# Performance work log

Measured on AMD Instinct MI355X. Metric: run time of the kernel, lower is better.

## Reference

```python
import jax, jax.numpy as jnp
import numpy as np
import math

INV = 1.0 / (2.0 * math.pi) ** 2  # 1/(2*pi)^2 normalization used throughout
EPS = 1e-8


def setup_inputs() -> dict:
    key = jax.random.key(0)
    ks = jax.random.split(key, 5)
    N, K, J = 512, 8, 6
    return {
        "x_hat": jax.random.normal(ks[0], (N, N, 2), jnp.float32),
        "phi_hat_real": jax.random.normal(ks[1], (N, N), jnp.float32),
        "phi_hat_imag": jax.random.normal(ks[2], (N, N), jnp.float32),
        "psi_hat_real": jax.random.normal(ks[3], (K, J, N, N), jnp.float32),
        "psi_hat_imag": jax.random.normal(ks[4], (K, J, N, N), jnp.float32),
    }


def reference(x_hat, phi_hat_real, phi_hat_imag, psi_hat_real, psi_hat_imag):
    K, J, N, _ = psi_hat_real.shape
    NN = N * N
    phi2 = phi_hat_real ** 2 + phi_hat_imag ** 2  # [N,N]

    # zeroth-order coefficient: full spatial mean of |x_hat|^2 * |phi_hat|^2
    s0 = INV * jnp.mean((x_hat[:, :, 0] ** 2 + x_hat[:, :, 1] ** 2) * phi2)

    # first layer: complex multiply in Fourier domain, ifft2, modulus, fft2
    xc = jax.lax.complex(x_hat[:, :, 0], x_hat[:, :, 1])          # [N,N] complex
    psic = jax.lax.complex(psi_hat_real, psi_hat_imag)            # [K,J,N,N] complex
    temp = jnp.fft.ifft2(xc[None, None] * psic, axes=(-2, -1))    # [K,J,N,N] complex
    mod = jnp.sqrt(temp.real ** 2 + temp.imag ** 2 + EPS)         # modulus nonlinearity
    t2 = jnp.fft.fft2(mod, axes=(-2, -1))                         # rfft onesided=False == full fft of real
    power = (t2.real ** 2 + t2.imag ** 2).reshape(K, J, NN)       # |U1_hat|^2

    # first-order coefficients a[k,i] = INV * mean(power * phi2)
    a = INV * (power @ phi2.reshape(NN)) / NN                     # [K,J]

    # second-order coefficients via GEMM over spatial dim:
    # B[k,i,m,j] = INV * mean_xy(power[k,i] * |psi[m,j]|^2)
    psi2 = (psi_hat_real ** 2 + psi_hat_imag ** 2).reshape(K, J, NN)
    B = INV * jnp.einsum('kin,mjn->kimj', power, psi2) / NN       # [K,J,K,J]

    # assemble output in the same concatenation order as the torch loop:
    # [s0, a_0, b_0(flattened over k,m,j'), a_1, b_1, ..., a_{J-1}]
    pieces = [s0[None]]
    for i in range(J):
        pieces.append(a[:, i])
        if i < J - 1:
            pieces.append(B[:, i, :, i + 1:J].reshape(-1))
    return jnp.concatenate(pieces, axis=0)
```

## Files before the change

kernel.cpp:

```cpp
#include <hip/hip_runtime.h>
#include <hip/hip_fp16.h>

#define Nn 512
#define NNe 262144
#define CST 546

__device__ __forceinline__ float2 f2(float x, float y){ return make_float2(x, y); }
__device__ __forceinline__ float2 cadd(float2 a, float2 b){ return f2(a.x+b.x, a.y+b.y); }
__device__ __forceinline__ float2 csub(float2 a, float2 b){ return f2(a.x-b.x, a.y-b.y); }
__device__ __forceinline__ float2 cmul(float2 a, float2 b){
    return f2(a.x*b.x - a.y*b.y, a.x*b.y + a.y*b.x);
}
__device__ __forceinline__ int pidx(int p){ return p + (p>>4) + (p>>7); }
#define WFENCE() __builtin_amdgcn_wave_barrier()

template<int SGN>
__device__ __forceinline__ void fft8(float2 a[8]){
    const float r = 0.7071067811865476f;
    const float S = (float)SGN;
    float2 u0 = cadd(a[0], a[4]), u1 = cadd(a[1], a[5]);
    float2 u2 = cadd(a[2], a[6]), u3 = cadd(a[3], a[7]);
    float2 v0 = csub(a[0], a[4]), v1 = csub(a[1], a[5]);
    float2 v2 = csub(a[2], a[6]), v3 = csub(a[3], a[7]);
    v1 = cmul(v1, f2(r, S*r));
    v2 = cmul(v2, f2(0.f, S));
    v3 = cmul(v3, f2(-r, S*r));
    float2 p0 = cadd(u0, u2), p1 = cadd(u1, u3);
    float2 q0 = csub(u0, u2), q1 = cmul(csub(u1, u3), f2(0.f, S));
    a[0] = cadd(p0, p1); a[4] = csub(p0, p1);
    a[2] = cadd(q0, q1); a[6] = csub(q0, q1);
    p0 = cadd(v0, v2); p1 = cadd(v1, v3);
    q0 = csub(v0, v2); q1 = cmul(csub(v1, v3), f2(0.f, S));
    a[1] = cadd(p0, p1); a[5] = csub(p0, p1);
    a[3] = cadd(q0, q1); a[7] = csub(q0, q1);
}

template<int SGN>
__device__ __forceinline__ float2 twd(int idx, float inv){
    float ang = ((float)SGN) * 6.283185307179586f * (inv * (float)idx);
    float s, c;
    __sincosf(ang, &s, &c);
    return f2(c, s);
}

template<int SGN>
__device__ void fft512_dif(float2 v[8], float2* buf, int lane){
    fft8<SGN>(v);
    {
        float2 w1 = twd<SGN>(lane, 1.f/512.f);
        float2 w  = f2(1.f, 0.f);
        #pragma unroll
        for (int r = 0; r < 8; ++r){
            buf[pidx(r*64 + lane)] = cmul(v[r], w);
            w = cmul(w, w1);
        }
    }
    WFENCE();
    int rb = (lane >> 3) * 64, t2 = lane & 7;
    float2 y[8];
    #pragma unroll
    for (int q = 0; q < 8; ++q) y[q] = buf[pidx(rb + t2 + 8*q)];
    fft8<SGN>(y);
    WFENCE();
    {
        float2 w2 = twd<SGN>(t2, 1.f/64.f);
        float2 w  = f2(1.f, 0.f);
        #pragma unroll
        for (int r = 0; r < 8; ++r){
            buf[pidx(rb + r*8 + t2)] = cmul(y[r], w);
            w = cmul(w, w2);
        }
    }
    WFENCE();
    int base = rb + t2*8;
    #pragma unroll
    for (int q = 0; q < 8; ++q) v[q] = buf[pidx(base + q)];
    fft8<SGN>(v);
}

template<int SGN>
__device__ void fft512_dit(float2 v[8], float2* buf, int lane){
    int rb = (lane >> 3) * 64, t2 = lane & 7;
    fft8<SGN>(v);
    int base = rb + t2*8;
    #pragma unroll
    for (int q = 0; q < 8; ++q) buf[pidx(base + q)] = v[q];
    WFENCE();
    float2 y[8];
    #pragma unroll
    for (int r = 0; r < 8; ++r) y[r] = buf[pidx(rb + r*8 + t2)];
    {
        float2 w2 = twd<SGN>(t2, 1.f/64.f);
        float2 w  = f2(1.f, 0.f);
        #pragma unroll
        for (int r = 0; r < 8; ++r){
            y[r] = cmul(y[r], w);
            w = cmul(w, w2);
        }
    }
    fft8<SGN>(y);
    WFENCE();
    #pragma unroll
    for (int q = 0; q < 8; ++q) buf[pidx(rb + t2 + 8*q)] = y[q];
    WFENCE();
    #pragma unroll
    for (int r = 0; r < 8; ++r) v[r] = buf[pidx(r*64 + lane)];
    {
        float2 w1 = twd<SGN>(lane, 1.f/512.f);
        float2 w  = f2(1.f, 0.f);
        #pragma unroll
        for (int r = 0; r < 8; ++r){
            v[r] = cmul(v[r], w);
            w = cmul(w, w1);
        }
    }
    fft8<SGN>(v);
}

__global__ __launch_bounds__(256, 6)
void k_mulrow(const float2* __restrict__ xh, const float* __restrict__ pr,
              const float* __restrict__ pi, __half2* __restrict__ temp,
              __half* __restrict__ psi2h){
    __shared__ float2 lds[4][548];
    int wave = threadIdx.x >> 6, lane = threadIdx.x & 63;
    int img  = blockIdx.x >> 7;
    int row  = ((blockIdx.x & 127) << 2) | wave;
    size_t boff = (size_t)img * NNe + (size_t)row * Nn;
    const float2* xr = xh + (size_t)row * Nn;
    float2 v[8];
    #pragma unroll
    for (int q = 0; q < 8; ++q){
        int x = lane + 64*q;
        float2 xv = xr[x];
        float2 pv = f2(pr[boff + x], pi[boff + x]);
        psi2h[boff + x] = __float2half_rn(pv.x*pv.x + pv.y*pv.y);
        v[q] = cmul(xv, pv);
    }
    fft512_dif<1>(v, lds[wave], lane);
    __half2* outp = temp + boff;
    #pragma unroll
    for (int q = 0; q < 8; ++q) outp[64*q + lane] = __floats2half2_rn(v[q].x, v[q].y);
}

__global__ __launch_bounds__(512, 6)
void k_colfused(__half2* __restrict__ temp){
    __shared__ float2 tile[8 * CST];
    int img = blockIdx.x >> 6;
    int x0  = (blockIdx.x & 63) << 3;
    __half2* srcH = temp + (size_t)img * NNe + x0;
    for (int i = threadIdx.x; i < 1024; i += 512){
        int yy = i >> 1, c4 = (i & 1) << 2;
        uint4 u = *(const uint4*)&srcH[(size_t)yy * Nn + c4];
        tile[(c4+0)*CST + pidx(yy)] = __half22float2(*(__half2*)&u.x);
        tile[(c4+1)*CST + pidx(yy)] = __half22float2(*(__half2*)&u.y);
        tile[(c4+2)*CST + pidx(yy)] = __half22float2(*(__half2*)&u.z);
        tile[(c4+3)*CST + pidx(yy)] = __half22float2(*(__half2*)&u.w);
    }
    __syncthreads();
    int wave = threadIdx.x >> 6, lane = threadIdx.x & 63;
    const float sc = 3.814697265625e-06f;
    {
        float2* buf = &tile[wave * CST];
        float2 v[8];
        #pragma unroll
        for (int q = 0; q < 8; ++q) v[q] = buf[pidx(lane + 64*q)];
        fft512_dif<1>(v, buf, lane);
        #pragma unroll
        for (int q = 0; q < 8; ++q){
            float re = v[q].x * sc, im = v[q].y * sc;
            v[q] = f2(sqrtf(re*re + im*im + 1e-8f), 0.f);
        }
        WFENCE();
        fft512_dit<-1>(v, buf, lane);
        #pragma unroll
        for (int q = 0; q < 8; ++q) buf[pidx(lane + 64*q)] = v[q];
    }
    __syncthreads();
    for (int i = threadIdx.x; i < 1024; i += 512){
        int yy = i >> 1, c4 = (i & 1) << 2;
        uint4 u;
        float2 a0 = tile[(c4+0)*CST + pidx(yy)];
        float2 a1 = tile[(c4+1)*CST + pidx(yy)];
        float2 a2 = tile[(c4+2)*CST + pidx(yy)];
        float2 a3 = tile[(c4+3)*CST + pidx(yy)];
        *(__half2*)&u.x = __floats2half2_rn(a0.x, a0.y);
        *(__half2*)&u.y = __floats2half2_rn(a1.x, a1.y);
        *(__half2*)&u.z = __floats2half2_rn(a2.x, a2.y);
        *(__half2*)&u.w = __floats2half2_rn(a3.x, a3.y);
        *(uint4*)&srcH[(size_t)yy * Nn + c4] = u;
    }
}

__global__ __launch_bounds__(256, 6)
void k_rowpow(const __half2* __restrict__ temp, __half* __restrict__ powerh){
    __shared__ float2 lds[4][548];
    int wave = threadIdx.x >> 6, lane = threadIdx.x & 63;
    int img  = blockIdx.x >> 7;
    int row  = ((blockIdx.x & 127) << 2) | wave;
    const __half2* src = temp + (size_t)img * NNe + (size_t)row * Nn;
    float2 v[8];
    #pragma unroll
    for (int q = 0; q < 8; ++q) v[q] = __half22float2(src[64*q + lane]);
    fft512_dit<-1>(v, lds[wave], lane);
    __half* dst = powerh + (size_t)img * NNe + (size_t)row * Nn;
    #pragma unroll
    for (int q = 0; q < 8; ++q)
        dst[lane + 64*q] = __float2half_rn((v[q].x*v[q].x + v[q].y*v[q].y) * 0.00390625f);
}

__global__ __launch_bounds__(256)
void k_s0(const float2* __restrict__ xh, const float* __restrict__ phr,
          const float* __restrict__ phii, float* __restrict__ part){
    int gid = blockIdx.x*256 + threadIdx.x;
    float acc = 0.f;
    for (int n = gid; n < NNe; n += 256*256){
        float2 x = xh[n];
        float a = phr[n], b = phii[n];
        acc += (x.x*x.x + x.y*x.y) * (a*a + b*b);
    }
    #pragma unroll
    for (int o = 32; o > 0; o >>= 1) acc += __shfl_down(acc, o, 64);
    __shared__ float wsum[4];
    int wave = threadIdx.x >> 6, lane = threadIdx.x & 63;
    if (lane == 0) wsum[wave] = acc;
    __syncthreads();
    if (threadIdx.x == 0) part[blockIdx.x] = wsum[0]+wsum[1]+wsum[2]+wsum[3];
}

__global__ __launch_bounds__(128)
void k_gemm(const __half* __restrict__ powerh, const __half* __restrict__ psi2h,
            const float* __restrict__ phr, const float* __restrict__ phii,
            float* __restrict__ partC){
    __shared__ __align__(16) float P[2][48][68];
    __shared__ __align__(16) float W[2][56][68];
    int wave = threadIdx.x >> 6, lane = threadIdx.x & 63;
    float (*Pw)[68] = P[wave];
    float (*Ww)[68] = W[wave];
    int gw = blockIdx.x*2 + wave;
    int lm = lane >> 3, lw = lane & 7;
    float acc[6][7] = {};
    #pragma unroll
    for (int r = 49; r < 56; ++r){
        Ww[r][lane] = 0.f;
        if (lane < 4) Ww[r][64 + lane] = 0.f;
    }
    int n0 = gw * 256;
    for (int st = 0; st < 4; ++st){
        int nb = n0 + st*64;
        __syncthreads();
        #pragma unroll
        for (int rr = 0; rr < 12; ++rr){
            int row = rr*4 + (lane >> 4);
            int c4  = (lane & 15) * 4;
            size_t off = (size_t)row*NNe + nb + c4;
            const __half2* p2 = (const __half2*)&powerh[off];
            float2 f0 = __half22float2(p2[0]);
            float2 f1 = __half22float2(p2[1]);
            *(float4*)&Pw[row][c4] = make_float4(f0.x, f0.y, f1.x, f1.y);
        }
        #pragma unroll
        for (int rr = 0; rr < 12; ++rr){
            int row = rr*4 + (lane >> 4);
            int c4  = (lane & 15) * 4;
            size_t off = (size_t)row*NNe + nb + c4;
            const __half2* p2 = (const __half2*)&psi2h[off];
            float2 f0 = __half22float2(p2[0]);
            float2 f1 = __half22float2(p2[1]);
            *(float4*)&Ww[row][c4] = make_float4(f0.x, f0.y, f1.x, f1.y);
        }
        if (lane < 16){
            int c4 = lane * 4;
            float4 a = *(const float4*)&phr[nb + c4];
            float4 b = *(const float4*)&phii[nb + c4];
            float4 w4;
            w4.x = a.x*a.x + b.x*b.x; w4.y = a.y*a.y + b.y*b.y;
            w4.z = a.z*a.z + b.z*b.z; w4.w = a.w*a.w + b.w*b.w;
            *(float4*)&Ww[48][c4] = w4;
        }
        __syncthreads();
        #pragma unroll 2
        for (int nn = 0; nn < 64; nn += 4){
            float4 pa[6], wb[7];
            #pragma unroll
            for (int i = 0; i < 6; ++i) pa[i] = *(const float4*)&Pw[lm + 8*i][nn];
            #pragma unroll
            for (int j = 0; j < 7; ++j) wb[j] = *(const float4*)&Ww[lw + 8*j][nn];
            #pragma unroll
            for (int i = 0; i < 6; ++i)
                #pragma unroll
                for (int j = 0; j < 7; ++j){
                    float s = acc[i][j];
                    s = fmaf(pa[i].x, wb[j].x, s);
                    s = fmaf(pa[i].y, wb[j].y, s);
                    s = fmaf(pa[i].z, wb[j].z, s);
                    s = fmaf(pa[i].w, wb[j].w, s);
                    acc[i][j] = s;
                }
        }
    }
    float* outp = partC + (size_t)gw * 2400;
    #pragma unroll
    for (int i = 0; i < 6; ++i)
        #pragma unroll
        for (int j = 0; j < 7; ++j){
            int m = lm + 8*i, wc = lw + 8*j;
            if (wc < 49) outp[m*50 + wc] = acc[i][j];
        }
}

__global__ __launch_bounds__(256)
void k_redc1(const float* __restrict__ partC, float* __restrict__ partC2){
    __shared__ float red[4][64];
    int es = threadIdx.x & 63, wave = threadIdx.x >> 6;
    int e = blockIdx.x*64 + es;
    int b0 = blockIdx.y*64 + wave*16;
    float s = 0.f;
    if (e < 2400){
        #pragma unroll
        for (int u = 0; u < 16; ++u) s += partC[(size_t)(b0+u)*2400 + e];
    }
    red[wave][es] = s;
    __syncthreads();
    if (wave == 0 && e < 2400)
        partC2[(size_t)blockIdx.y*2400 + e] = red[0][es]+red[1][es]+red[2][es]+red[3][es];
}
__global__ __launch_bounds__(256)
void k_redc2(const float* __restrict__ partC2, float* __restrict__ CF){
    __shared__ float red[4][64];
    int es = threadIdx.x & 63, wave = threadIdx.x >> 6;
    int e = blockIdx.x*64 + es;
    float s = 0.f;
    if (e < 2400){
        #pragma unroll
        for (int u = 0; u < 4; ++u) s += partC2[(size_t)(wave*4+u)*2400 + e];
    }
    red[wave][es] = s;
    __syncthreads();
    if (wave == 0 && e < 2400)
        CF[e] = red[0][es]+red[1][es]+red[2][es]+red[3][es];
}

__global__ __launch_bounds__(256)
void k_final(const float* __restrict__ CF, const float* __restrict__ partS0,
             float* __restrict__ outp, float SC0, float SCC){
    __shared__ float ssum[4];
    int tid = threadIdx.x, wave = tid >> 6, lane = tid & 63;
    float a = partS0[tid];
    #pragma unroll
    for (int o = 32; o > 0; o >>= 1) a += __shfl_down(a, o, 64);
    if (lane == 0) ssum[wave] = a;
    __syncthreads();
    if (tid == 0) outp[0] = SC0 * (ssum[0]+ssum[1]+ssum[2]+ssum[3]);
    int off = 1;
    for (int i = 0; i < 6; ++i){
        if (tid < 8) outp[off + tid] = SCC * CF[(tid*6 + i)*50 + 48];
        off += 8;
        if (i < 5){
            int nj = 5 - i, cnt = 64 * nj;
            for (int p = tid; p < cnt; p += 256){
                int j2 = p % nj;
                int km = p / nj;
                int m = km & 7, k = km >> 3;
                outp[off + p] = SCC * CF[(k*6 + i)*50 + m*6 + (i + 1 + j2)];
            }
            off += cnt;
        }
    }
}

extern "C" void kernel_launch(void* const* d_in, const int* in_sizes, int n_in,
                              void* d_out, int out_size, void* d_ws, size_t ws_size,
                              hipStream_t stream){
    (void)in_sizes; (void)n_in; (void)out_size; (void)ws_size;
    const float2* xh  = (const float2*)d_in[0];
    const float*  phr = (const float*)d_in[1];
    const float*  phi_= (const float*)d_in[2];
    const float*  psr = (const float*)d_in[3];
    const float*  psi_= (const float*)d_in[4];
    float* outp = (float*)d_out;
    float* ws   = (float*)d_ws;

    size_t o_power = 0;
    size_t o_partC = o_power + (size_t)24 * NNe;
    size_t o_pC2   = o_partC + (size_t)1024 * 2400;
    size_t o_s0    = o_pC2 + (size_t)16 * 2400;
    size_t o_CF    = o_s0 + 256;
    size_t o_temp  = o_CF + 2400;
    size_t o_psi2  = o_temp + (size_t)48 * NNe;
    __half*  powerh= (__half*)(ws + o_power);
    float*   partC = ws + o_partC;
    float*   partC2= ws + o_pC2;
    float*   ps0   = ws + o_s0;
    float*   CF    = ws + o_CF;
    __half2* temp  = (__half2*)(ws + o_temp);
    __half*  psi2h = (__half*)(ws + o_psi2);

    const double INVd = 1.0 / (4.0 * 3.14159265358979323846 * 3.14159265358979323846);
    const float SC0 = (float)(INVd / (double)NNe);
    const float SCC = (float)(INVd / (double)NNe * 256.0);

    k_s0<<<dim3(256), dim3(256), 0, stream>>>(xh, phr, phi_, ps0);
    k_mulrow<<<dim3(48*128), dim3(256), 0, stream>>>(xh, psr, psi_, temp, psi2h);
    k_colfused<<<dim3(48*64), dim3(512), 0, stream>>>(temp);
    k_rowpow<<<dim3(48*128), dim3(256), 0, stream>>>(temp, powerh);
    k_gemm<<<dim3(512), dim3(128), 0, stream>>>(powerh, psi2h, phr, phi_, partC);
    k_redc1<<<dim3(38, 16), dim3(256), 0, stream>>>(partC, partC2);
    k_redc2<<<dim3(38), dim3(256), 0, stream>>>(partC2, CF);
    k_final<<<dim3(1), dim3(256), 0, stream>>>(CF, ps0, outp, SC0, SCC);
}
```

Baseline: 158.2 us.

## Precompute FFT twiddles, relax GEMM barriers, fold final reduction into output kernel

The row-FFT kernels now compute their twiddle tables once per lane and reuse them through the radix stages, using conjugation for the inverse sign instead of separate sincos calls. In the GEMM kernel, block-wide barriers around the per-step LDS staging become wave-level barriers, which assumes each wave touches only its own LDS region. The second partial-sum reduction kernel is removed and its 16-way sum moves into the final output kernel through shared memory, saving one launch and a global round trip. The barrier change risks a race if the staged tiles are shared across waves.

```diff
diff --git a/kernel.cpp b/kernel.cpp
--- a/kernel.cpp
+++ b/kernel.cpp
@@ -35,19 +35,84 @@
     a[3] = cadd(q0, q1); a[7] = csub(q0, q1);
 }
 
-template<int SGN>
-__device__ __forceinline__ float2 twd(int idx, float inv){
-    float ang = ((float)SGN) * 6.283185307179586f * (inv * (float)idx);
+__device__ __forceinline__ float2 twdp(int idx, float inv){
+    float ang = 6.283185307179586f * (inv * (float)idx);
     float s, c;
     __sincosf(ang, &s, &c);
     return f2(c, s);
 }
 
 template<int SGN>
-__device__ void fft512_dif(float2 v[8], float2* buf, int lane){
+__device__ __forceinline__ float2 applyw(float2 a, float2 w){
+    return (SGN > 0) ? f2(a.x*w.x - a.y*w.y, a.x*w.y + a.y*w.x)
+                     : f2(a.x*w.x + a.y*w.y, a.y*w.x - a.x*w.y);
+}
+
+__device__ __forceinline__ void make_tw(int lane, float2 tw1[8], float2 tw2[8]){
+    tw1[0] = f2(1.f, 0.f); tw1[1] = twdp(lane, 1.f/512.f);
+    #pragma unroll
+    for (int r = 2; r < 8; ++r) tw1[r] = cmul(tw1[r-1], tw1[1]);
+    tw2[0] = f2(1.f, 0.f); tw2[1] = twdp(lane & 7, 1.f/64.f);
+    #pragma unroll
+    for (int r = 2; r < 8; ++r) tw2[r] = cmul(tw2[r-1], tw2[1]);
+}
+
+template<int SGN>
+__device__ void fft512_dif(float2 v[8], float2* buf, int lane,
+                           const float2 tw1[8], const float2 tw2[8]){
+    fft8<SGN>(v);
+    #pragma unroll
+    for (int r = 0; r < 8; ++r)
+        buf[pidx(r*64 + lane)] = applyw<SGN>(v[r], tw1[r]);
+    WFENCE();
+    int rb = (lane >> 3) * 64, t2 = lane & 7;
+    float2 y[8];
+    #pragma unroll
+    for (int q = 0; q < 8; ++q) y[q] = buf[pidx(rb + t2 + 8*q)];
+    fft8<SGN>(y);
+    WFENCE();
+    #pragma unroll
+    for (int r = 0; r < 8; ++r)
+        buf[pidx(rb + r*8 + t2)] = applyw<SGN>(y[r], tw2[r]);
+    WFENCE();
+    int base = rb + t2*8;
+    #pragma unroll
+    for (int q = 0; q < 8; ++q) v[q] = buf[pidx(base + q)];
+    fft8<SGN>(v);
+}
+
+template<int SGN>
+__device__ void fft512_dit(float2 v[8], float2* buf, int lane,
+                           const float2 tw1[8], const float2 tw2[8]){
+    int rb = (lane >> 3) * 64, t2 = lane & 7;
+    fft8<SGN>(v);
+    int base = rb + t2*8;
+    #pragma unroll
+    for (int q = 0; q < 8; ++q) buf[pidx(base + q)] = v[q];
+    WFENCE();
+    float2 y[8];
+    #pragma unroll
+    for (int r = 0; r < 8; ++r) y[r] = buf[pidx(rb + r*8 + t2)];
+    #pragma unroll
+    for (int r = 0; r < 8; ++r) y[r] = applyw<SGN>(y[r], tw2[r]);
+    fft8<SGN>(y);
+    WFENCE();
+    #pragma unroll
+    for (int q = 0; q < 8; ++q) buf[pidx(rb + t2 + 8*q)] = y[q];
+    WFENCE();
+    #pragma unroll
+    for (int r = 0; r < 8; ++r) v[r] = buf[pidx(r*64 + lane)];
+    #pragma unroll
+    for (int r = 0; r < 8; ++r) v[r] = applyw<SGN>(v[r], tw1[r]);
+    fft8<SGN>(v);
+}
+
+template<int SGN>
+__device__ void fft512_dif_i(float2 v[8], float2* buf, int lane){
     fft8<SGN>(v);
     {
-        float2 w1 = twd<SGN>(lane, 1.f/512.f);
+        float2 w1 = twdp(lane, 1.f/512.f);
+        if (SGN < 0) w1.y = -w1.y;
         float2 w  = f2(1.f, 0.f);
         #pragma unroll
         for (int r = 0; r < 8; ++r){
@@ -63,7 +128,8 @@
     fft8<SGN>(y);
     WFENCE();
     {
-        float2 w2 = twd<SGN>(t2, 1.f/64.f);
+        float2 w2 = twdp(t2, 1.f/64.f);
+        if (SGN < 0) w2.y = -w2.y;
         float2 w  = f2(1.f, 0.f);
         #pragma unroll
         for (int r = 0; r < 8; ++r){
@@ -79,7 +145,7 @@
 }
 
 template<int SGN>
-__device__ void fft512_dit(float2 v[8], float2* buf, int lane){
+__device__ void fft512_dit_i(float2 v[8], float2* buf, int lane){
     int rb = (lane >> 3) * 64, t2 = lane & 7;
     fft8<SGN>(v);
     int base = rb + t2*8;
@@ -90,7 +156,8 @@
     #pragma unroll
     for (int r = 0; r < 8; ++r) y[r] = buf[pidx(rb + r*8 + t2)];
     {
-        float2 w2 = twd<SGN>(t2, 1.f/64.f);
+        float2 w2 = twdp(t2, 1.f/64.f);
+        if (SGN < 0) w2.y = -w2.y;
         float2 w  = f2(1.f, 0.f);
         #pragma unroll
         for (int r = 0; r < 8; ++r){
@@ -106,7 +173,8 @@
     #pragma unroll
     for (int r = 0; r < 8; ++r) v[r] = buf[pidx(r*64 + lane)];
     {
-        float2 w1 = twd<SGN>(lane, 1.f/512.f);
+        float2 w1 = twdp(lane, 1.f/512.f);
+        if (SGN < 0) w1.y = -w1.y;
         float2 w  = f2(1.f, 0.f);
         #pragma unroll
         for (int r = 0; r < 8; ++r){
@@ -125,6 +193,8 @@
     int wave = threadIdx.x >> 6, lane = threadIdx.x & 63;
     int img  = blockIdx.x >> 7;
     int row  = ((blockIdx.x & 127) << 2) | wave;
+    float2 tw1[8], tw2[8];
+    make_tw(lane, tw1, tw2);
     size_t boff = (size_t)img * NNe + (size_t)row * Nn;
     const float2* xr = xh + (size_t)row * Nn;
     float2 v[8];
@@ -136,7 +206,7 @@
         psi2h[boff + x] = __float2half_rn(pv.x*pv.x + pv.y*pv.y);
         v[q] = cmul(xv, pv);
     }
-    fft512_dif<1>(v, lds[wave], lane);
+    fft512_dif<1>(v, lds[wave], lane, tw1, tw2);
     __half2* outp = temp + boff;
     #pragma unroll
     for (int q = 0; q < 8; ++q) outp[64*q + lane] = __floats2half2_rn(v[q].x, v[q].y);
@@ -164,14 +234,14 @@
         float2 v[8];
         #pragma unroll
         for (int q = 0; q < 8; ++q) v[q] = buf[pidx(lane + 64*q)];
-        fft512_dif<1>(v, buf, lane);
+        fft512_dif_i<1>(v, buf, lane);
         #pragma unroll
         for (int q = 0; q < 8; ++q){
             float re = v[q].x * sc, im = v[q].y * sc;
             v[q] = f2(sqrtf(re*re + im*im + 1e-8f), 0.f);
         }
         WFENCE();
-        fft512_dit<-1>(v, buf, lane);
+        fft512_dit_i<-1>(v, buf, lane);
         #pragma unroll
         for (int q = 0; q < 8; ++q) buf[pidx(lane + 64*q)] = v[q];
     }
@@ -197,11 +267,13 @@
     int wave = threadIdx.x >> 6, lane = threadIdx.x & 63;
     int img  = blockIdx.x >> 7;
     int row  = ((blockIdx.x & 127) << 2) | wave;
+    float2 tw1[8], tw2[8];
+    make_tw(lane, tw1, tw2);
     const __half2* src = temp + (size_t)img * NNe + (size_t)row * Nn;
     float2 v[8];
     #pragma unroll
     for (int q = 0; q < 8; ++q) v[q] = __half22float2(src[64*q + lane]);
-    fft512_dit<-1>(v, lds[wave], lane);
+    fft512_dit<-1>(v, lds[wave], lane, tw1, tw2);
     __half* dst = powerh + (size_t)img * NNe + (size_t)row * Nn;
     #pragma unroll
     for (int q = 0; q < 8; ++q)
@@ -247,7 +319,7 @@
     int n0 = gw * 256;
     for (int st = 0; st < 4; ++st){
         int nb = n0 + st*64;
-        __syncthreads();
+        WFENCE();
         #pragma unroll
         for (int rr = 0; rr < 12; ++rr){
             int row = rr*4 + (lane >> 4);
@@ -277,7 +349,7 @@
             w4.z = a.z*a.z + b.z*b.z; w4.w = a.w*a.w + b.w*b.w;
             *(float4*)&Ww[48][c4] = w4;
         }
-        __syncthreads();
+        WFENCE();
         #pragma unroll 2
         for (int nn = 0; nn < 64; nn += 4){
             float4 pa[6], wb[7];
@@ -324,27 +396,19 @@
     if (wave == 0 && e < 2400)
         partC2[(size_t)blockIdx.y*2400 + e] = red[0][es]+red[1][es]+red[2][es]+red[3][es];
 }
+
 __global__ __launch_bounds__(256)
-void k_redc2(const float* __restrict__ partC2, float* __restrict__ CF){
-    __shared__ float red[4][64];
-    int es = threadIdx.x & 63, wave = threadIdx.x >> 6;
-    int e = blockIdx.x*64 + es;
-    float s = 0.f;
-    if (e < 2400){
-        #pragma unroll
-        for (int u = 0; u < 4; ++u) s += partC2[(size_t)(wave*4+u)*2400 + e];
-    }
-    red[wave][es] = s;
-    __syncthreads();
-    if (wave == 0 && e < 2400)
-        CF[e] = red[0][es]+red[1][es]+red[2][es]+red[3][es];
-}
-
-__global__ __launch_bounds__(256)
-void k_final(const float* __restrict__ CF, const float* __restrict__ partS0,
+void k_final(const float* __restrict__ partC2, const float* __restrict__ partS0,
              float* __restrict__ outp, float SC0, float SCC){
+    __shared__ float CFs[2400];
     __shared__ float ssum[4];
     int tid = threadIdx.x, wave = tid >> 6, lane = tid & 63;
+    for (int e = tid; e < 2400; e += 256){
+        float s = 0.f;
+        #pragma unroll
+        for (int u = 0; u < 16; ++u) s += partC2[(size_t)u*2400 + e];
+        CFs[e] = SCC * s;
+    }
     float a = partS0[tid];
     #pragma unroll
     for (int o = 32; o > 0; o >>= 1) a += __shfl_down(a, o, 64);
@@ -353,7 +417,7 @@
     if (tid == 0) outp[0] = SC0 * (ssum[0]+ssum[1]+ssum[2]+ssum[3]);
     int off = 1;
     for (int i = 0; i < 6; ++i){
-        if (tid < 8) outp[off + tid] = SCC * CF[(tid*6 + i)*50 + 48];
+        if (tid < 8) outp[off + tid] = CFs[(tid*6 + i)*50 + 48];
         off += 8;
         if (i < 5){
             int nj = 5 - i, cnt = 64 * nj;
@@ -361,7 +425,7 @@
                 int j2 = p % nj;
                 int km = p / nj;
                 int m = km & 7, k = km >> 3;
-                outp[off + p] = SCC * CF[(k*6 + i)*50 + m*6 + (i + 1 + j2)];
+                outp[off + p] = CFs[(k*6 + i)*50 + m*6 + (i + 1 + j2)];
             }
             off += cnt;
         }
@@ -384,14 +448,12 @@
     size_t o_partC = o_power + (size_t)24 * NNe;
     size_t o_pC2   = o_partC + (size_t)1024 * 2400;
     size_t o_s0    = o_pC2 + (size_t)16 * 2400;
-    size_t o_CF    = o_s0 + 256;
-    size_t o_temp  = o_CF + 2400;
+    size_t o_temp  = o_s0 + 256;
     size_t o_psi2  = o_temp + (size_t)48 * NNe;
     __half*  powerh= (__half*)(ws + o_power);
     float*   partC = ws + o_partC;
     float*   partC2= ws + o_pC2;
     float*   ps0   = ws + o_s0;
-    float*   CF    = ws + o_CF;
     __half2* temp  = (__half2*)(ws + o_temp);
     __half*  psi2h = (__half*)(ws + o_psi2);
 
@@ -405,6 +467,5 @@
     k_rowpow<<<dim3(48*128), dim3(256), 0, stream>>>(temp, powerh);
     k_gemm<<<dim3(512), dim3(128), 0, stream>>>(powerh, psi2h, phr, phi_, partC);
     k_redc1<<<dim3(38, 16), dim3(256), 0, stream>>>(partC, partC2);
-    k_redc2<<<dim3(38), dim3(256), 0, stream>>>(partC2, CF);
-    k_final<<<dim3(1), dim3(256), 0, stream>>>(CF, ps0, outp, SC0, SCC);
-}
+    k_final<<<dim3(1), dim3(256), 0, stream>>>(partC2, ps0, outp, SC0, SCC);
+}
```

Measured after the change: 162.6 us. 2.8% more time.
